# Optimization experiments

Hardware: AMD Instinct MI355X
Metric: run time of the kernel (lower is better)

Reference implementation:

```python
import jax, jax.numpy as jnp
from jax import lax
import numpy as np

T, N, E = 8, 20000, 640000
D_IN, H, K = 2, 64, 3


def setup_inputs() -> dict:
    key = jax.random.key(0)
    ks = jax.random.split(key, 10)
    x = jax.random.normal(ks[0], (T, N, D_IN), dtype=jnp.float32)
    edge_idx = jax.random.randint(ks[1], (T, 2, E), 0, N, dtype=jnp.int64)
    edge_attr = jax.random.uniform(ks[2], (T, E), dtype=jnp.float32)
    Fin = D_IN + H
    s = 0.05
    Wr = jax.random.normal(ks[3], (K, Fin, H), dtype=jnp.float32) * s
    Wu = jax.random.normal(ks[4], (K, Fin, H), dtype=jnp.float32) * s
    Wc = jax.random.normal(ks[5], (K, Fin, H), dtype=jnp.float32) * s
    br = jnp.zeros((H,), dtype=jnp.float32)
    bu = jnp.zeros((H,), dtype=jnp.float32)
    bc = jnp.zeros((H,), dtype=jnp.float32)
    return {"x": x, "edge_idx": edge_idx, "edge_attr": edge_attr,
            "Wr": Wr, "br": br, "Wu": Wu, "bu": bu, "Wc": Wc, "bc": bc}


def reference(x, edge_idx, edge_attr, Wr, br, Wu, bu, Wc, bc):
    n = x.shape[1]
    k_hops = Wr.shape[0]

    def cheb(v, src, dst, wn, W, b):
        # Chebyshev recursion on scaled Laplacian (PyG ChebConv, lambda_max=2)
        def prop(t):
            return jax.ops.segment_sum(wn[:, None] * t[src], dst, num_segments=n)
        Tx0 = v
        out = Tx0 @ W[0]
        Tx1 = prop(Tx0)
        out = out + Tx1 @ W[1]
        for kk in range(2, k_hops):
            Tx2 = 2.0 * prop(Tx1) - Tx0
            out = out + Tx2 @ W[kk]
            Tx0, Tx1 = Tx1, Tx2
        return out + b

    def step(h, inp):
        x_t, ei, w_t = inp
        src, dst = ei[0], ei[1]
        # sym-normalized Laplacian, scaled by 2/lambda_max=1; self-loop weight is 0
        deg = jax.ops.segment_sum(w_t, src, num_segments=n)
        safe = jnp.where(deg > 0, deg, 1.0)
        dinv = jnp.where(deg > 0, lax.rsqrt(safe), 0.0)
        wn = -dinv[src] * w_t * dinv[dst]
        comb = jnp.concatenate([x_t, h], axis=1)
        r = jax.nn.sigmoid(cheb(comb, src, dst, wn, Wr, br))
        u = jax.nn.sigmoid(cheb(comb, src, dst, wn, Wu, bu))
        c = jnp.tanh(cheb(jnp.concatenate([x_t, r * h], axis=1), src, dst, wn, Wc, bc))
        h_new = u * h + (1.0 - u) * c
        return h_new, None

    h0 = jnp.zeros((n, br.shape[0]), dtype=x.dtype)
    h_final, _ = lax.scan(step, h0, (x, edge_idx, edge_attr))
    return h_final
```

## Files before the change

### kernel.cpp

```cpp
#include <hip/hip_runtime.h>

#define NN 20000
#define EE 640000
#define TT 8
#define HF 64
#define AS 232
#define ACS 104
#define BSS 194
#define PBLK 5000
#define TILE 2560
#define NBIN 250
#define BWID 80
#define ECAP 3072
#define LCAP 24
#define DCH 128

typedef _Float16 f16;
typedef unsigned int uint;
typedef __attribute__((ext_vector_type(8))) _Float16 half8;
typedef __attribute__((ext_vector_type(4))) float floatx4;

__device__ __forceinline__ float lo16f(uint v) { return (float)__builtin_bit_cast(f16, (unsigned short)(v & 0xffff)); }
__device__ __forceinline__ float hi16f(uint v) { return (float)__builtin_bit_cast(f16, (unsigned short)(v >> 16)); }
__device__ __forceinline__ uint pk16(float a, float b) {
    unsigned short ua = __builtin_bit_cast(unsigned short, (f16)a);
    unsigned short ub = __builtin_bit_cast(unsigned short, (f16)b);
    return (uint)ua | ((uint)ub << 16);
}

__global__ __launch_bounds__(256) void k_prepW(
    const float* __restrict__ Wr, const float* __restrict__ Wu, const float* __restrict__ Wc,
    f16* __restrict__ Wp, f16* __restrict__ Wcp)
{
    int idx = blockIdx.x * 256 + threadIdx.x;
    if (idx < 8 * 7 * 64) {
        int lane = idx & 63;
        int kb = (idx >> 6) % 7;
        int nb = (idx >> 6) / 7;
        int col = nb * 16 + (lane & 15);
        int g = col >> 6, jj = col & 63;
        const float* W = (g == 0) ? Wr : Wu;
        half8 v;
        #pragma unroll
        for (int e = 0; e < 8; e++) {
            int k = kb * 32 + ((lane >> 4) << 3) + e;
            float val = 0.f;
            if (k < 192)      { int hop = k >> 6; int i = 2 + (k & 63); val = W[(hop * 66 + i) * 64 + jj]; }
            else if (k < 198) { int q = k - 192;  int hop = q >> 1;     val = W[(hop * 66 + (q & 1)) * 64 + jj]; }
            v[e] = (f16)val;
        }
        *(half8*)&Wp[(size_t)idx * 8] = v;
        return;
    }
    int idx2 = idx - 8 * 7 * 64;
    if (idx2 >= 12 * 3 * 64) return;
    int lane = idx2 & 63;
    int kb = (idx2 >> 6) % 3;
    int nbc = (idx2 >> 6) / 3;
    int col = nbc * 16 + (lane & 15);
    int mode = col >> 6, j = col & 63;
    half8 v;
    #pragma unroll
    for (int e = 0; e < 8; e++) {
        int k = kb * 32 + ((lane >> 4) << 3) + e;
        float val = 0.f;
        if (k < 66) {
            if (mode == 0)      val = Wc[(0 * 66 + k) * 64 + j] - Wc[(2 * 66 + k) * 64 + j];
            else if (mode == 1) val = Wc[(1 * 66 + k) * 64 + j];
            else                val = Wc[(2 * 66 + k) * 64 + j];
        }
        v[e] = (f16)val;
    }
    *(half8*)&Wcp[(size_t)idx2 * 8] = v;
}

__global__ __launch_bounds__(256) void k_deg(
    const int* __restrict__ eidx, const float* __restrict__ eatt, int t0,
    float* __restrict__ deg)
{
    __shared__ float dl[NN];
    int tl = blockIdx.x >> 7, chunk = blockIdx.x & (DCH - 1);
    int tid = threadIdx.x;
    for (int n = tid; n < NN; n += 256) dl[n] = 0.f;
    __syncthreads();
    const int*   src = eidx + (size_t)(t0 + tl) * 2 * EE + chunk * (EE / DCH);
    const float* w   = eatt + (size_t)(t0 + tl) * EE + chunk * (EE / DCH);
    for (int e = tid; e < EE / DCH; e += 256) {
        int s = __builtin_nontemporal_load(&src[e]);
        float wv = __builtin_nontemporal_load(&w[e]);
        atomicAdd(&dl[s], wv);
    }
    __syncthreads();
    float* dg = deg + (size_t)tl * NN;
    for (int n = tid; n < NN; n += 256) {
        float v = dl[n];
        if (v != 0.f) atomicAdd(&dg[n], v);
    }
}

__global__ __launch_bounds__(256) void k_dinv_setx(
    float* __restrict__ deg, float* __restrict__ dinv,
    const float* __restrict__ x4, uint* __restrict__ xf4, int* __restrict__ binptr)
{
    int idx = blockIdx.x * 256 + threadIdx.x;
    if (idx < 4 * NBIN) binptr[idx] = 0;
    if (idx >= 4 * NN) return;
    float d = deg[idx];
    deg[idx] = 0.f;
    dinv[idx] = d > 0.f ? 1.f / sqrtf(d) : 0.f;
    int tl = idx / NN, n = idx - tl * NN;
    xf4[idx] = pk16(x4[(size_t)tl * NN * 2 + 2 * n], x4[(size_t)tl * NN * 2 + 2 * n + 1]);
}

__global__ __launch_bounds__(256) void k_bin(
    const int* __restrict__ eidx, const float* __restrict__ eatt, int t0,
    int* __restrict__ binptr, uint2* __restrict__ ebuf)
{
    __shared__ uint2 buf[NBIN][LCAP];
    __shared__ int lcnt[NBIN];
    __shared__ int scan[256];
    __shared__ int gb[NBIN];
    int tid = threadIdx.x;
    if (tid < NBIN) lcnt[tid] = 0;
    __syncthreads();
    int tl = blockIdx.x / 250, tile = blockIdx.x % 250;
    const int*   src = eidx + (size_t)(t0 + tl) * 2 * EE + tile * TILE;
    const int*   dst = src + EE;
    const float* w   = eatt + (size_t)(t0 + tl) * EE + tile * TILE;
    int* bp = binptr + tl * NBIN;
    size_t ebase = (size_t)tl * NBIN * ECAP;
    #pragma unroll
    for (int i = 0; i < TILE / 256; i++) {
        int e = i * 256 + tid;
        int s = __builtin_nontemporal_load(&src[e]);
        int d = __builtin_nontemporal_load(&dst[e]);
        float wv = __builtin_nontemporal_load(&w[e]);
        int bin = d / BWID;
        uint2 ent = make_uint2(((uint)d << 16) | (uint)s, __float_as_uint(wv));
        int p = atomicAdd(&lcnt[bin], 1);
        if (p < LCAP) buf[bin][p] = ent;
        else {
            int gp = atomicAdd(&bp[bin], 1);
            if (gp < ECAP) ebuf[ebase + (size_t)bin * ECAP + gp] = ent;
        }
    }
    __syncthreads();
    int c = (tid < NBIN) ? (lcnt[tid] < LCAP ? lcnt[tid] : LCAP) : 0;
    scan[tid] = c;
    __syncthreads();
    #pragma unroll
    for (int o = 1; o < 256; o <<= 1) {
        int v = (tid >= o) ? scan[tid - o] : 0;
        __syncthreads();
        scan[tid] += v;
        __syncthreads();
    }
    if (c > 0) gb[tid] = atomicAdd(&bp[tid], c);
    __syncthreads();
    int total = scan[255];
    for (int i = tid; i < total; i += 256) {
        int lo = 0, hi = 255;
        #pragma unroll
        for (int it = 0; it < 8; it++) { int mid = (lo + hi) >> 1; if (scan[mid] > i) hi = mid; else lo = mid + 1; }
        int p = i - (lo ? scan[lo - 1] : 0);
        int gp = gb[lo] + p;
        if (gp < ECAP) ebuf[ebase + (size_t)lo * ECAP + gp] = buf[lo][p];
    }
}

__global__ __launch_bounds__(256) void k_csr(
    const uint2* __restrict__ ebuf, const int* __restrict__ binptr,
    const float* __restrict__ dinv,
    uint* __restrict__ entries, int* __restrict__ row_ptr, int* __restrict__ cnt)
{
    __shared__ uint proc[ECAP];
    __shared__ unsigned char lnb[ECAP];
    __shared__ uint staged[ECAP];
    __shared__ int lcnt[BWID], loff[BWID];
    int tl = blockIdx.x / NBIN, b = blockIdx.x % NBIN, tid = threadIdx.x;
    int nume = binptr[tl * NBIN + b]; if (nume > ECAP) nume = ECAP;
    const float* dv = dinv + (size_t)tl * NN;
    size_t base = (size_t)(tl * NBIN + b) * ECAP;
    if (tid < BWID) lcnt[tid] = 0;
    __syncthreads();
    for (int i = tid; i < nume; i += 256) {
        uint2 ent = ebuf[base + i];
        int s = ent.x & 0xffff;
        int d = ent.x >> 16;
        float wv = __uint_as_float(ent.y);
        float wn = -dv[s] * wv * dv[d];
        unsigned short wb = __builtin_bit_cast(unsigned short, (f16)wn);
        proc[i] = ((uint)wb << 16) | (uint)s;
        int ln = d - b * BWID;
        lnb[i] = (unsigned char)ln;
        atomicAdd(&lcnt[ln], 1);
    }
    __syncthreads();
    if (tid == 0) {
        int run = 0;
        for (int i = 0; i < BWID; i++) { loff[i] = run; run += lcnt[i]; }
    }
    __syncthreads();
    if (tid < BWID) {
        int n = tl * NN + b * BWID + tid;
        row_ptr[n] = (int)base + loff[tid];
        cnt[n] = lcnt[tid];
    }
    __syncthreads();
    for (int i = tid; i < nume; i += 256) {
        int p = atomicAdd(&loff[lnb[i]], 1);
        staged[p] = proc[i];
    }
    __syncthreads();
    for (int i = tid; i < nume; i += 256)
        entries[base + i] = staged[i];
}

__device__ __forceinline__ void gather64(
    const f16* __restrict__ src_mat, const uint* wnb, int mp, int j, int q,
    float& s0, float& s1)
{
    float acc0[8], acc1[8];
    #pragma unroll
    for (int k = 0; k < 8; k++) { acc0[k] = 0.f; acc1[k] = 0.f; }
    for (int e = 0; e < mp; e += 16) {
        uint ee[8], rr[8];
        #pragma unroll
        for (int k = 0; k < 8; k++) ee[k] = wnb[e + 2 * k + q];
        #pragma unroll
        for (int k = 0; k < 8; k++) rr[k] = *(const uint*)&src_mat[(size_t)(ee[k] & 0xffff) * HF + 2 * j];
        #pragma unroll
        for (int k = 0; k < 8; k++) {
            float w = hi16f(ee[k]);
            acc0[k] += w * lo16f(rr[k]);
            acc1[k] += w * hi16f(rr[k]);
        }
    }
    s0 = ((acc0[0] + acc0[1]) + (acc0[2] + acc0[3])) + ((acc0[4] + acc0[5]) + (acc0[6] + acc0[7]));
    s1 = ((acc1[0] + acc1[1]) + (acc1[2] + acc1[3])) + ((acc1[4] + acc1[5]) + (acc1[6] + acc1[7]));
    s0 += __shfl_xor(s0, 32);
    s1 += __shfl_xor(s1, 32);
}

__global__ __launch_bounds__(256) void k_prop(
    const f16* __restrict__ src_mat, const f16* __restrict__ base,
    f16* __restrict__ dst,
    const int* __restrict__ row_ptr, const int* __restrict__ cnt,
    const uint* __restrict__ entries,
    float alpha, float beta,
    const uint* __restrict__ xsrc, const uint* __restrict__ xbase,
    uint* __restrict__ xdst)
{
    __shared__ uint wnbuf[4][128];
    int ws = threadIdx.x >> 6, lane = threadIdx.x & 63;
    int node = blockIdx.x * 4 + ws;
    int m = cnt[node]; if (m > 128) m = 128;
    int st = row_ptr[node];
    int mp = (m + 15) & ~15;
    for (int idx = lane; idx < mp; idx += 64)
        wnbuf[ws][idx] = (idx < m) ? entries[st + idx] : 0u;
    asm volatile("s_waitcnt lgkmcnt(0)" ::: "memory");

    int j = lane & 31, q = lane >> 5;
    float s0, s1;
    gather64(src_mat, wnbuf[ws], mp, j, q, s0, s1);
    if (q == 0) {
        float r0 = alpha * s0, r1 = alpha * s1;
        if (base) {
            uint bv = *(const uint*)&base[(size_t)node * HF + 2 * j];
            r0 += beta * lo16f(bv);
            r1 += beta * hi16f(bv);
        }
        *(uint*)&dst[(size_t)node * HF + 2 * j] = pk16(r0, r1);
    }

    if (xdst) {
        float xa0 = 0.f, xa1 = 0.f;
        for (int i = lane; i < mp; i += 64) {
            uint ent = wnbuf[ws][i];
            uint xv = xsrc[ent & 0xffff];
            float wn = hi16f(ent);
            xa0 += wn * lo16f(xv);
            xa1 += wn * hi16f(xv);
        }
        #pragma unroll
        for (int o = 32; o >= 1; o >>= 1) {
            xa0 += __shfl_xor(xa0, o);
            xa1 += __shfl_xor(xa1, o);
        }
        if (lane == 0) {
            float r0 = alpha * xa0, r1 = alpha * xa1;
            if (xbase) { uint bv = xbase[node]; r0 += beta * lo16f(bv); r1 += beta * hi16f(bv); }
            xdst[node] = pk16(r0, r1);
        }
    }
}

__global__ __launch_bounds__(256) void k_prop_fin(
    const f16* __restrict__ S, const f16* __restrict__ B0,
    const f16* __restrict__ u, const float* __restrict__ h_in,
    float* __restrict__ h_out, f16* __restrict__ hA_out,
    const int* __restrict__ row_ptr, const int* __restrict__ cnt,
    const uint* __restrict__ entries)
{
    __shared__ uint wnbuf[4][128];
    int ws = threadIdx.x >> 6, lane = threadIdx.x & 63;
    int node = blockIdx.x * 4 + ws;
    int m = cnt[node]; if (m > 128) m = 128;
    int st = row_ptr[node];
    int mp = (m + 15) & ~15;
    for (int idx = lane; idx < mp; idx += 64)
        wnbuf[ws][idx] = (idx < m) ? entries[st + idx] : 0u;
    asm volatile("s_waitcnt lgkmcnt(0)" ::: "memory");

    int j = lane & 31, q = lane >> 5;
    float s0, s1;
    gather64(S, wnbuf[ws], mp, j, q, s0, s1);
    if (q == 0) {
        uint b0v = *(const uint*)&B0[(size_t)node * HF + 2 * j];
        float c0 = tanhf(s0 + lo16f(b0v));
        float c1 = tanhf(s1 + hi16f(b0v));
        uint uv = *(const uint*)&u[(size_t)node * HF + 2 * j];
        float u0 = lo16f(uv), u1 = hi16f(uv);
        float2 hv = *(const float2*)&h_in[(size_t)node * HF + 2 * j];
        float hn0 = u0 * hv.x + (1.f - u0) * c0;
        float hn1 = u1 * hv.y + (1.f - u1) * c1;
        *(float2*)&h_out[(size_t)node * HF + 2 * j] = make_float2(hn0, hn1);
        *(uint*)&hA_out[(size_t)node * HF + 2 * j] = pk16(hn0, hn1);
    }
}

#define MFMA16(a, b, c) __builtin_amdgcn_mfma_f32_16x16x32_f16(a, b, c, 0, 0, 0)

__global__ __launch_bounds__(512) void k_ru(
    const f16* __restrict__ hA, const f16* __restrict__ t1, const f16* __restrict__ t2,
    const uint* __restrict__ xf, const uint* __restrict__ t1x, const uint* __restrict__ t2x,
    const f16* __restrict__ Wp, const f16* __restrict__ Wcp,
    const float* __restrict__ br, const float* __restrict__ bu, const float* __restrict__ bc,
    f16* __restrict__ u_out,
    f16* __restrict__ B0, f16* __restrict__ B1, f16* __restrict__ B2)
{
    __shared__ __attribute__((aligned(16))) f16 At[64][AS];
    __shared__ __attribute__((aligned(16))) f16 Ac[64][ACS];
    __shared__ f16 Ub[64][68];
    int n0 = blockIdx.x * 64;
    int tid = threadIdx.x;

    for (int idx = tid; idx < 64 * 8 * 3; idx += 512) {
        int a = idx >> 9, r = (idx >> 3) & 63, s = idx & 7;
        const f16* src = (a == 0) ? hA : (a == 1 ? t1 : t2);
        int gn = n0 + r;
        half8 v = {0, 0, 0, 0, 0, 0, 0, 0};
        if (gn < NN) v = *(const half8*)&src[(size_t)gn * HF + s * 8];
        *(half8*)&At[r][a * 64 + s * 8] = v;
    }
    for (int idx = tid; idx < 64 * 17; idx += 512) {
        int r = idx / 17, c = idx % 17;
        *(uint*)((char*)&At[r][198] + 4 * c) = 0u;
    }
    for (int idx = tid; idx < 64 * 3; idx += 512) {
        int r = idx & 63, a = idx >> 6;
        const uint* src = (a == 0) ? xf : (a == 1 ? t1x : t2x);
        int gn = n0 + r;
        uint v = 0;
        if (gn < NN) v = src[gn];
        *(uint*)&At[r][192 + 2 * a] = v;
    }
    for (int idx = tid; idx < 64; idx += 512) {
        int gn = n0 + idx;
        *(uint*)&Ac[idx][0] = (gn < NN) ? xf[gn] : 0u;
    }
    for (int idx = tid; idx < 64 * 15; idx += 512) {
        int r = idx / 15, c = idx % 15;
        *(uint*)((char*)&Ac[r][66] + 4 * c) = 0u;
    }
    __syncthreads();

    int wid = tid >> 6, lane = tid & 63;
    int mrow = (wid & 1) * 32;
    int nb0 = (wid >> 1) * 2;
    int arow = mrow + (lane & 15);
    int koff = (lane >> 4) << 3;
    floatx4 z = {0.f, 0.f, 0.f, 0.f};
    {
        floatx4 acc00 = z, acc01 = z, acc10 = z, acc11 = z;
        #pragma unroll
        for (int kb = 0; kb < 7; kb++) {
            half8 a0 = *(const half8*)&At[arow][kb * 32 + koff];
            half8 a1 = *(const half8*)&At[arow + 16][kb * 32 + koff];
            half8 b0 = *(const half8*)&Wp[(size_t)(((nb0    ) * 7 + kb) * 64 + lane) * 8];
            half8 b1 = *(const half8*)&Wp[(size_t)(((nb0 + 1) * 7 + kb) * 64 + lane) * 8];
            acc00 = MFMA16(a0, b0, acc00);
            acc10 = MFMA16(a1, b0, acc10);
            acc01 = MFMA16(a0, b1, acc01);
            acc11 = MFMA16(a1, b1, acc11);
        }
        bool isR = nb0 < 4;
        #pragma unroll
        for (int mi = 0; mi < 2; mi++) {
            #pragma unroll
            for (int ni = 0; ni < 2; ni++) {
                floatx4 a = (mi == 0) ? (ni == 0 ? acc00 : acc01) : (ni == 0 ? acc10 : acc11);
                int jj = ((nb0 + ni) * 16 + (lane & 15)) & 63;
                float bias = isR ? br[jj] : bu[jj];
                int rbase = mrow + mi * 16 + ((lane >> 4) << 2);
                #pragma unroll
                for (int e = 0; e < 4; e++) {
                    int rloc = rbase + e;
                    float s = 1.f / (1.f + __expf(-(a[e] + bias)));
                    if (isR) {
                        float hv = (float)At[rloc][jj];
                        Ac[rloc][2 + jj] = (f16)(s * hv);
                    } else {
                        Ub[rloc][jj] = (f16)s;
                    }
                }
            }
        }
    }
    __syncthreads();

    for (int idx = tid; idx < 64 * 32; idx += 512) {
        int n = idx >> 5, c = idx & 31;
        int gn = n0 + n;
        if (gn < NN) *(uint*)&u_out[(size_t)gn * HF + 2 * c] = *(uint*)&Ub[n][2 * c];
    }
    f16* Bs = &At[0][0];
    #pragma unroll
    for (int i = 0; i < 6; i++) {
        int t = wid * 6 + i;
        int nbc = t >> 2, mq = t & 3;
        int ar = mq * 16 + (lane & 15);
        floatx4 acc;
        float binit = (nbc < 4) ? bc[nbc * 16 + (lane & 15)] : 0.f;
        acc[0] = binit; acc[1] = binit; acc[2] = binit; acc[3] = binit;
        #pragma unroll
        for (int kb = 0; kb < 3; kb++) {
            half8 a = *(const half8*)&Ac[ar][kb * 32 + koff];
            half8 b = *(const half8*)&Wcp[(size_t)(((nbc * 3 + kb) * 64) + lane) * 8];
            acc = MFMA16(a, b, acc);
        }
        int rbase = mq * 16 + ((lane >> 4) << 2);
        int col = nbc * 16 + (lane & 15);
        #pragma unroll
        for (int e = 0; e < 4; e++)
            Bs[(size_t)(rbase + e) * BSS + col] = (f16)acc[e];
    }
    __syncthreads();

    for (int idx = tid; idx < 64 * 96; idx += 512) {
        int n = idx / 96, c = idx % 96;
        int gn = n0 + n;
        if (gn < NN) {
            int col = 2 * c;
            f16* Bdst = (col < 64) ? B0 : (col < 128 ? B1 : B2);
            *(uint*)&Bdst[(size_t)gn * HF + (col & 63)] = *(uint*)&Bs[(size_t)n * BSS + col];
        }
    }
}


extern "C" void kernel_launch(void* const* d_in, const int* in_sizes, int n_in,
                              void* d_out, int out_size, void* d_ws, size_t ws_size,
                              hipStream_t stream)
{
    const float* x    = (const float*)d_in[0];
    const int*   eidx = (const int*)d_in[1];
    const float* eatt = (const float*)d_in[2];
    const float* Wr   = (const float*)d_in[3];
    const float* br   = (const float*)d_in[4];
    const float* Wu   = (const float*)d_in[5];
    const float* bu   = (const float*)d_in[6];
    const float* Wc   = (const float*)d_in[7];
    const float* bc   = (const float*)d_in[8];

    char* ws = (char*)d_ws;
    size_t off = 0;
    auto alloc = [&](size_t bytes) -> void* {
        void* p = ws + off;
        off += (bytes + 255) & ~(size_t)255;
        return p;
    };
    const size_t FB = (size_t)NN * HF * 2;
    float* h_f32  = (float*)alloc((size_t)NN * HF * 4);
    f16*   hA     = (f16*)alloc(FB);
    f16*   t1     = (f16*)alloc(FB);
    f16*   t2     = (f16*)alloc(FB);
    f16*   u      = (f16*)alloc(FB);
    f16*   B0     = (f16*)alloc(FB);
    f16*   B1     = (f16*)alloc(FB);
    f16*   B2     = (f16*)alloc(FB);
    float* deg    = (float*)alloc((size_t)4 * NN * 4);
    float* dinv   = (float*)alloc((size_t)4 * NN * 4);
    uint*  xf     = (uint*)alloc((size_t)TT * NN * 4);
    uint*  t1x    = (uint*)alloc((size_t)NN * 4);
    uint*  t2x    = (uint*)alloc((size_t)NN * 4);
    int*   binptr = (int*)alloc((size_t)4 * NBIN * 4);
    uint2* ebuf   = (uint2*)alloc((size_t)4 * NBIN * ECAP * 8);
    uint*  entr   = (uint*)alloc((size_t)4 * NBIN * ECAP * 4);
    int*   rowp   = (int*)alloc((size_t)4 * NN * 4);
    int*   cnt    = (int*)alloc((size_t)4 * NN * 4);
    f16*   Wp     = (f16*)alloc((size_t)8 * 7 * 64 * 8 * 2);
    f16*   Wcp    = (f16*)alloc((size_t)12 * 3 * 64 * 8 * 2);

    hipMemsetAsync(h_f32, 0, (size_t)NN * HF * 4 + FB, stream);
    hipMemsetAsync(deg, 0, (size_t)4 * NN * 4, stream);
    k_prepW<<<30, 256, 0, stream>>>(Wr, Wu, Wc, Wp, Wcp);

    const int GB = (NN + 63) / 64;
    const int DB = (4 * NN + 255) / 256;

    for (int half = 0; half < 2; ++half) {
        int t0 = half * 4;
        k_deg      <<<4 * DCH, 256, 0, stream>>>(eidx, eatt, t0, deg);
        k_dinv_setx<<<DB, 256, 0, stream>>>(deg, dinv,
                                            x + (size_t)t0 * NN * 2, xf + (size_t)t0 * NN, binptr);
        k_bin      <<<1000, 256, 0, stream>>>(eidx, eatt, t0, binptr, ebuf);
        k_csr      <<<1000, 256, 0, stream>>>(ebuf, binptr, dinv, entr, rowp, cnt);

        for (int tl = 0; tl < 4; ++tl) {
            int t = t0 + tl;
            const int* rp = rowp + (size_t)tl * NN;
            const int* cp = cnt + (size_t)tl * NN;
            uint* xft = xf + (size_t)t * NN;

            k_prop<<<PBLK, 256, 0, stream>>>(hA, nullptr, t1, rp, cp, entr, 1.f,  0.f, xft, nullptr, t1x);
            k_prop<<<PBLK, 256, 0, stream>>>(t1, hA,      t2, rp, cp, entr, 2.f, -1.f, t1x, xft,     t2x);

            k_ru<<<GB, 512, 0, stream>>>(hA, t1, t2, xft, t1x, t2x, Wp, Wcp,
                                         br, bu, bc, u, B0, B1, B2);

            k_prop<<<PBLK, 256, 0, stream>>>(B2, B1, t2, rp, cp, entr, 2.f, 1.f, nullptr, nullptr, nullptr);

            float* hdst = (t == TT - 1) ? (float*)d_out : h_f32;
            k_prop_fin<<<PBLK, 256, 0, stream>>>(t2, B0, u, h_f32, hdst, hA, rp, cp, entr);
        }
    }
}
```

Measured before the change: 760.8 us.

## Fuse degree computation into binning pass and widen gather unroll to 32

Removes the separate degree kernel, which re-read all source indices and weights and zeroed a 20000-float shared array per block. The binning kernel now also bins edges by source node into a second buffer (edge weight stored as fp16), and a new per-bin reduction kernel computes dinv from those bins. The gather loop in propagation now processes 32 edges per iteration instead of 16, raising memory-level parallelism at the cost of more padding and more registers. Degrees are now accumulated from fp16-rounded weights, which slightly changes precision, and the larger register footprint could reduce occupancy.

```diff
diff --git a/kernel.cpp b/kernel.cpp
--- a/kernel.cpp
+++ b/kernel.cpp
@@ -13,7 +13,6 @@
 #define BWID 80
 #define ECAP 3072
 #define LCAP 24
-#define DCH 128
 
 typedef _Float16 f16;
 typedef unsigned int uint;
@@ -74,60 +73,36 @@
     *(half8*)&Wcp[(size_t)idx2 * 8] = v;
 }
 
-__global__ __launch_bounds__(256) void k_deg(
-    const int* __restrict__ eidx, const float* __restrict__ eatt, int t0,
-    float* __restrict__ deg)
-{
-    __shared__ float dl[NN];
-    int tl = blockIdx.x >> 7, chunk = blockIdx.x & (DCH - 1);
-    int tid = threadIdx.x;
-    for (int n = tid; n < NN; n += 256) dl[n] = 0.f;
-    __syncthreads();
-    const int*   src = eidx + (size_t)(t0 + tl) * 2 * EE + chunk * (EE / DCH);
-    const float* w   = eatt + (size_t)(t0 + tl) * EE + chunk * (EE / DCH);
-    for (int e = tid; e < EE / DCH; e += 256) {
-        int s = __builtin_nontemporal_load(&src[e]);
-        float wv = __builtin_nontemporal_load(&w[e]);
-        atomicAdd(&dl[s], wv);
-    }
-    __syncthreads();
-    float* dg = deg + (size_t)tl * NN;
-    for (int n = tid; n < NN; n += 256) {
-        float v = dl[n];
-        if (v != 0.f) atomicAdd(&dg[n], v);
-    }
-}
-
-__global__ __launch_bounds__(256) void k_dinv_setx(
-    float* __restrict__ deg, float* __restrict__ dinv,
-    const float* __restrict__ x4, uint* __restrict__ xf4, int* __restrict__ binptr)
+__global__ __launch_bounds__(256) void k_setx(
+    const float* __restrict__ x4, uint* __restrict__ xf4,
+    int* __restrict__ binptr, int* __restrict__ sbinptr)
 {
     int idx = blockIdx.x * 256 + threadIdx.x;
-    if (idx < 4 * NBIN) binptr[idx] = 0;
+    if (idx < 4 * NBIN) { binptr[idx] = 0; sbinptr[idx] = 0; }
     if (idx >= 4 * NN) return;
-    float d = deg[idx];
-    deg[idx] = 0.f;
-    dinv[idx] = d > 0.f ? 1.f / sqrtf(d) : 0.f;
     int tl = idx / NN, n = idx - tl * NN;
     xf4[idx] = pk16(x4[(size_t)tl * NN * 2 + 2 * n], x4[(size_t)tl * NN * 2 + 2 * n + 1]);
 }
 
 __global__ __launch_bounds__(256) void k_bin(
     const int* __restrict__ eidx, const float* __restrict__ eatt, int t0,
-    int* __restrict__ binptr, uint2* __restrict__ ebuf)
+    int* __restrict__ binptr, uint2* __restrict__ ebuf,
+    int* __restrict__ sbinptr, uint* __restrict__ sbuf)
 {
     __shared__ uint2 buf[NBIN][LCAP];
-    __shared__ int lcnt[NBIN];
+    __shared__ uint  sbl[NBIN][LCAP];
+    __shared__ int lcnt[NBIN], scnt[NBIN];
     __shared__ int scan[256];
     __shared__ int gb[NBIN];
     int tid = threadIdx.x;
-    if (tid < NBIN) lcnt[tid] = 0;
+    if (tid < NBIN) { lcnt[tid] = 0; scnt[tid] = 0; }
     __syncthreads();
     int tl = blockIdx.x / 250, tile = blockIdx.x % 250;
     const int*   src = eidx + (size_t)(t0 + tl) * 2 * EE + tile * TILE;
     const int*   dst = src + EE;
     const float* w   = eatt + (size_t)(t0 + tl) * EE + tile * TILE;
     int* bp = binptr + tl * NBIN;
+    int* sp = sbinptr + tl * NBIN;
     size_t ebase = (size_t)tl * NBIN * ECAP;
     #pragma unroll
     for (int i = 0; i < TILE / 256; i++) {
@@ -143,28 +118,83 @@
             int gp = atomicAdd(&bp[bin], 1);
             if (gp < ECAP) ebuf[ebase + (size_t)bin * ECAP + gp] = ent;
         }
-    }
-    __syncthreads();
-    int c = (tid < NBIN) ? (lcnt[tid] < LCAP ? lcnt[tid] : LCAP) : 0;
-    scan[tid] = c;
-    __syncthreads();
-    #pragma unroll
-    for (int o = 1; o < 256; o <<= 1) {
-        int v = (tid >= o) ? scan[tid - o] : 0;
+        int sbin = s / BWID;
+        uint sent = (pk16(wv, 0.f) << 16) | (uint)s;
+        int sq = atomicAdd(&scnt[sbin], 1);
+        if (sq < LCAP) sbl[sbin][sq] = sent;
+        else {
+            int gp = atomicAdd(&sp[sbin], 1);
+            if (gp < ECAP) sbuf[ebase + (size_t)sbin * ECAP + gp] = sent;
+        }
+    }
+    __syncthreads();
+    {
+        int c = (tid < NBIN) ? (lcnt[tid] < LCAP ? lcnt[tid] : LCAP) : 0;
+        scan[tid] = c;
         __syncthreads();
-        scan[tid] += v;
+        #pragma unroll
+        for (int o = 1; o < 256; o <<= 1) {
+            int v = (tid >= o) ? scan[tid - o] : 0;
+            __syncthreads();
+            scan[tid] += v;
+            __syncthreads();
+        }
+        if (c > 0) gb[tid] = atomicAdd(&bp[tid], c);
         __syncthreads();
-    }
-    if (c > 0) gb[tid] = atomicAdd(&bp[tid], c);
-    __syncthreads();
-    int total = scan[255];
-    for (int i = tid; i < total; i += 256) {
-        int lo = 0, hi = 255;
-        #pragma unroll
-        for (int it = 0; it < 8; it++) { int mid = (lo + hi) >> 1; if (scan[mid] > i) hi = mid; else lo = mid + 1; }
-        int p = i - (lo ? scan[lo - 1] : 0);
-        int gp = gb[lo] + p;
-        if (gp < ECAP) ebuf[ebase + (size_t)lo * ECAP + gp] = buf[lo][p];
+        int total = scan[255];
+        for (int i = tid; i < total; i += 256) {
+            int lo = 0, hi = 255;
+            #pragma unroll
+            for (int it = 0; it < 8; it++) { int mid = (lo + hi) >> 1; if (scan[mid] > i) hi = mid; else lo = mid + 1; }
+            int p = i - (lo ? scan[lo - 1] : 0);
+            int gp = gb[lo] + p;
+            if (gp < ECAP) ebuf[ebase + (size_t)lo * ECAP + gp] = buf[lo][p];
+        }
+    }
+    __syncthreads();
+    {
+        int c = (tid < NBIN) ? (scnt[tid] < LCAP ? scnt[tid] : LCAP) : 0;
+        scan[tid] = c;
+        __syncthreads();
+        #pragma unroll
+        for (int o = 1; o < 256; o <<= 1) {
+            int v = (tid >= o) ? scan[tid - o] : 0;
+            __syncthreads();
+            scan[tid] += v;
+            __syncthreads();
+        }
+        if (c > 0) gb[tid] = atomicAdd(&sp[tid], c);
+        __syncthreads();
+        int total = scan[255];
+        for (int i = tid; i < total; i += 256) {
+            int lo = 0, hi = 255;
+            #pragma unroll
+            for (int it = 0; it < 8; it++) { int mid = (lo + hi) >> 1; if (scan[mid] > i) hi = mid; else lo = mid + 1; }
+            int p = i - (lo ? scan[lo - 1] : 0);
+            int gp = gb[lo] + p;
+            if (gp < ECAP) sbuf[ebase + (size_t)lo * ECAP + gp] = sbl[lo][p];
+        }
+    }
+}
+
+__global__ __launch_bounds__(256) void k_degred(
+    const uint* __restrict__ sbuf, const int* __restrict__ sbinptr,
+    float* __restrict__ dinv)
+{
+    __shared__ float dacc[BWID];
+    int tl = blockIdx.x / NBIN, b = blockIdx.x % NBIN, tid = threadIdx.x;
+    int nume = sbinptr[tl * NBIN + b]; if (nume > ECAP) nume = ECAP;
+    if (tid < BWID) dacc[tid] = 0.f;
+    __syncthreads();
+    size_t base = (size_t)(tl * NBIN + b) * ECAP;
+    for (int i = tid; i < nume; i += 256) {
+        uint e = sbuf[base + i];
+        atomicAdd(&dacc[(e & 0xffff) - b * BWID], hi16f(e));
+    }
+    __syncthreads();
+    if (tid < BWID) {
+        float d = dacc[tid];
+        dinv[(size_t)tl * NN + b * BWID + tid] = d > 0.f ? 1.f / sqrtf(d) : 0.f;
     }
 }
 
@@ -220,24 +250,24 @@
     const f16* __restrict__ src_mat, const uint* wnb, int mp, int j, int q,
     float& s0, float& s1)
 {
-    float acc0[8], acc1[8];
+    float a0[8], a1[8];
     #pragma unroll
-    for (int k = 0; k < 8; k++) { acc0[k] = 0.f; acc1[k] = 0.f; }
-    for (int e = 0; e < mp; e += 16) {
-        uint ee[8], rr[8];
-        #pragma unroll
-        for (int k = 0; k < 8; k++) ee[k] = wnb[e + 2 * k + q];
-        #pragma unroll
-        for (int k = 0; k < 8; k++) rr[k] = *(const uint*)&src_mat[(size_t)(ee[k] & 0xffff) * HF + 2 * j];
-        #pragma unroll
-        for (int k = 0; k < 8; k++) {
+    for (int k = 0; k < 8; k++) { a0[k] = 0.f; a1[k] = 0.f; }
+    for (int e = 0; e < mp; e += 32) {
+        uint ee[16], rr[16];
+        #pragma unroll
+        for (int k = 0; k < 16; k++) ee[k] = wnb[e + 2 * k + q];
+        #pragma unroll
+        for (int k = 0; k < 16; k++) rr[k] = *(const uint*)&src_mat[(size_t)(ee[k] & 0xffff) * HF + 2 * j];
+        #pragma unroll
+        for (int k = 0; k < 16; k++) {
             float w = hi16f(ee[k]);
-            acc0[k] += w * lo16f(rr[k]);
-            acc1[k] += w * hi16f(rr[k]);
-        }
-    }
-    s0 = ((acc0[0] + acc0[1]) + (acc0[2] + acc0[3])) + ((acc0[4] + acc0[5]) + (acc0[6] + acc0[7]));
-    s1 = ((acc1[0] + acc1[1]) + (acc1[2] + acc1[3])) + ((acc1[4] + acc1[5]) + (acc1[6] + acc1[7]));
+            a0[k & 7] += w * lo16f(rr[k]);
+            a1[k & 7] += w * hi16f(rr[k]);
+        }
+    }
+    s0 = ((a0[0] + a0[1]) + (a0[2] + a0[3])) + ((a0[4] + a0[5]) + (a0[6] + a0[7]));
+    s1 = ((a1[0] + a1[1]) + (a1[2] + a1[3])) + ((a1[4] + a1[5]) + (a1[6] + a1[7]));
     s0 += __shfl_xor(s0, 32);
     s1 += __shfl_xor(s1, 32);
 }
@@ -256,7 +286,7 @@
     int node = blockIdx.x * 4 + ws;
     int m = cnt[node]; if (m > 128) m = 128;
     int st = row_ptr[node];
-    int mp = (m + 15) & ~15;
+    int mp = (m + 31) & ~31;
     for (int idx = lane; idx < mp; idx += 64)
         wnbuf[ws][idx] = (idx < m) ? entries[st + idx] : 0u;
     asm volatile("s_waitcnt lgkmcnt(0)" ::: "memory");
@@ -308,7 +338,7 @@
     int node = blockIdx.x * 4 + ws;
     int m = cnt[node]; if (m > 128) m = 128;
     int st = row_ptr[node];
-    int mp = (m + 15) & ~15;
+    int mp = (m + 31) & ~31;
     for (int idx = lane; idx < mp; idx += 64)
         wnbuf[ws][idx] = (idx < m) ? entries[st + idx] : 0u;
     asm volatile("s_waitcnt lgkmcnt(0)" ::: "memory");
@@ -482,29 +512,29 @@
         return p;
     };
     const size_t FB = (size_t)NN * HF * 2;
-    float* h_f32  = (float*)alloc((size_t)NN * HF * 4);
-    f16*   hA     = (f16*)alloc(FB);
-    f16*   t1     = (f16*)alloc(FB);
-    f16*   t2     = (f16*)alloc(FB);
-    f16*   u      = (f16*)alloc(FB);
-    f16*   B0     = (f16*)alloc(FB);
-    f16*   B1     = (f16*)alloc(FB);
-    f16*   B2     = (f16*)alloc(FB);
-    float* deg    = (float*)alloc((size_t)4 * NN * 4);
-    float* dinv   = (float*)alloc((size_t)4 * NN * 4);
-    uint*  xf     = (uint*)alloc((size_t)TT * NN * 4);
-    uint*  t1x    = (uint*)alloc((size_t)NN * 4);
-    uint*  t2x    = (uint*)alloc((size_t)NN * 4);
-    int*   binptr = (int*)alloc((size_t)4 * NBIN * 4);
-    uint2* ebuf   = (uint2*)alloc((size_t)4 * NBIN * ECAP * 8);
-    uint*  entr   = (uint*)alloc((size_t)4 * NBIN * ECAP * 4);
-    int*   rowp   = (int*)alloc((size_t)4 * NN * 4);
-    int*   cnt    = (int*)alloc((size_t)4 * NN * 4);
-    f16*   Wp     = (f16*)alloc((size_t)8 * 7 * 64 * 8 * 2);
-    f16*   Wcp    = (f16*)alloc((size_t)12 * 3 * 64 * 8 * 2);
+    float* h_f32   = (float*)alloc((size_t)NN * HF * 4);
+    f16*   hA      = (f16*)alloc(FB);
+    f16*   t1      = (f16*)alloc(FB);
+    f16*   t2      = (f16*)alloc(FB);
+    f16*   u       = (f16*)alloc(FB);
+    f16*   B0      = (f16*)alloc(FB);
+    f16*   B1      = (f16*)alloc(FB);
+    f16*   B2      = (f16*)alloc(FB);
+    float* dinv    = (float*)alloc((size_t)4 * NN * 4);
+    uint*  xf      = (uint*)alloc((size_t)TT * NN * 4);
+    uint*  t1x     = (uint*)alloc((size_t)NN * 4);
+    uint*  t2x     = (uint*)alloc((size_t)NN * 4);
+    int*   binptr  = (int*)alloc((size_t)4 * NBIN * 4);
+    int*   sbinptr = (int*)alloc((size_t)4 * NBIN * 4);
+    uint2* ebuf    = (uint2*)alloc((size_t)4 * NBIN * ECAP * 8);
+    uint*  sbuf    = (uint*)alloc((size_t)4 * NBIN * ECAP * 4);
+    uint*  entr    = (uint*)alloc((size_t)4 * NBIN * ECAP * 4);
+    int*   rowp    = (int*)alloc((size_t)4 * NN * 4);
+    int*   cnt     = (int*)alloc((size_t)4 * NN * 4);
+    f16*   Wp      = (f16*)alloc((size_t)8 * 7 * 64 * 8 * 2);
+    f16*   Wcp     = (f16*)alloc((size_t)12 * 3 * 64 * 8 * 2);
 
     hipMemsetAsync(h_f32, 0, (size_t)NN * HF * 4 + FB, stream);
-    hipMemsetAsync(deg, 0, (size_t)4 * NN * 4, stream);
     k_prepW<<<30, 256, 0, stream>>>(Wr, Wu, Wc, Wp, Wcp);
 
     const int GB = (NN + 63) / 64;
@@ -512,11 +542,11 @@
 
     for (int half = 0; half < 2; ++half) {
         int t0 = half * 4;
-        k_deg      <<<4 * DCH, 256, 0, stream>>>(eidx, eatt, t0, deg);
-        k_dinv_setx<<<DB, 256, 0, stream>>>(deg, dinv,
-                                            x + (size_t)t0 * NN * 2, xf + (size_t)t0 * NN, binptr);
-        k_bin      <<<1000, 256, 0, stream>>>(eidx, eatt, t0, binptr, ebuf);
-        k_csr      <<<1000, 256, 0, stream>>>(ebuf, binptr, dinv, entr, rowp, cnt);
+        k_setx  <<<DB, 256, 0, stream>>>(x + (size_t)t0 * NN * 2, xf + (size_t)t0 * NN,
+                                         binptr, sbinptr);
+        k_bin   <<<1000, 256, 0, stream>>>(eidx, eatt, t0, binptr, ebuf, sbinptr, sbuf);
+        k_degred<<<1000, 256, 0, stream>>>(sbuf, sbinptr, dinv);
+        k_csr   <<<1000, 256, 0, stream>>>(ebuf, binptr, dinv, entr, rowp, cnt);
 
         for (int tl = 0; tl < 4; ++tl) {
             int t = t0 + tl;
```

After: 744.9 us. -2.1%, faster.
